# Kernel tuning notes

Measured on AMD Instinct MI355X. Metric: run time of the kernel, lower is better.

## Reference

```python
import jax, jax.numpy as jnp
import numpy as np

N_NODES = 100000


def gcn_conv(x, edge_index, W, b, n):
    """PyG-style GCNConv: h = D^-1/2 (A + I) D^-1/2 (x W) + b."""
    h = x @ W  # [n, out]
    loops = jnp.arange(n, dtype=edge_index.dtype)
    src = jnp.concatenate([edge_index[0], loops])
    dst = jnp.concatenate([edge_index[1], loops])
    deg = jax.ops.segment_sum(jnp.ones_like(dst, dtype=h.dtype), dst, num_segments=n)
    dinv = jnp.where(deg > 0, jax.lax.rsqrt(deg), 0.0)
    norm = dinv[src] * dinv[dst]  # [E+n]
    msg = h[src] * norm[:, None]
    out = jax.ops.segment_sum(msg, dst, num_segments=n)
    return out + b


def setup_inputs() -> dict:
    key = jax.random.key(0)
    ks = jax.random.split(key, 12)
    n, f, hid, c, e = N_NODES, 128, 16, 32, 3200000
    x = jax.random.normal(ks[0], (n, f), dtype=jnp.float32)
    edge_index_pos = jax.random.randint(ks[1], (2, e), 0, n, dtype=jnp.int32)
    edge_index_neg = jax.random.randint(ks[2], (2, e), 0, n, dtype=jnp.int32)
    def glorot(k, fi, fo):
        lim = np.sqrt(6.0 / (fi + fo)).astype(np.float32)
        return jax.random.uniform(k, (fi, fo), minval=-lim, maxval=lim, dtype=jnp.float32)
    return {
        "x": x,
        "edge_index_pos": edge_index_pos,
        "edge_index_neg": edge_index_neg,
        "W1p": glorot(ks[3], f, hid), "b1p": jnp.zeros((hid,), jnp.float32),
        "W1n": glorot(ks[4], f, hid), "b1n": jnp.zeros((hid,), jnp.float32),
        "W2p": glorot(ks[5], hid, c), "b2p": jnp.zeros((c,), jnp.float32),
        "W2n": glorot(ks[6], hid, c), "b2n": jnp.zeros((c,), jnp.float32),
    }


def reference(x, edge_index_pos, edge_index_neg, W1p, b1p, W1n, b1n, W2p, b2p, W2n, b2n):
    n = x.shape[0]
    # layer 1: relu(pos) - relu(neg)
    h = (jax.nn.relu(gcn_conv(x, edge_index_pos, W1p, b1p, n))
         - jax.nn.relu(gcn_conv(x, edge_index_neg, W1n, b1n, n)))
    # dropout is identity in eval mode (training=False)
    h = (jax.nn.relu(gcn_conv(h, edge_index_pos, W2p, b2p, n))
         - jax.nn.relu(gcn_conv(h, edge_index_neg, W2n, b2n, n)))
    return jax.nn.log_softmax(h, axis=1)
```

## Files before the change

kernel.cpp:

```cpp
#include <hip/hip_runtime.h>
#include <hip/hip_fp16.h>


#define BSHIFT 8
#define BSZ 256
#define MAX_NBK 512
#define FILL_CAP 13056
#define SORT_CAP 12032

typedef int   i32x4 __attribute__((ext_vector_type(4)));
typedef float f32x4 __attribute__((ext_vector_type(4)));

__device__ __forceinline__ int chunk_of_block(int bid, int NCH) {
  return (NCH % 8 == 0) ? (bid % 8) * (NCH / 8) + bid / 8 : bid;
}


__global__ __launch_bounds__(256) void bucket_count2(
    const int* __restrict__ eP, const int* __restrict__ eN,
    int E, int CH, int NCH, int NBK, int* __restrict__ ccP, int* __restrict__ ccN) {
  __shared__ int cnt[MAX_NBK];
  const int* dsts = (blockIdx.y ? eN : eP) + E;
  int* cc = blockIdx.y ? ccN : ccP;
  const int c = chunk_of_block(blockIdx.x, NCH);
  for (int i = threadIdx.x; i < NBK; i += 256) cnt[i] = 0;
  __syncthreads();
  int base = c * CH, end = min(E, base + CH);
  for (int idx = base + threadIdx.x * 4; idx < end; idx += 1024) {
    if (idx + 4 <= end) {
      i32x4 d = __builtin_nontemporal_load((const i32x4*)(dsts + idx));
      atomicAdd(&cnt[d.x >> BSHIFT], 1);
      atomicAdd(&cnt[d.y >> BSHIFT], 1);
      atomicAdd(&cnt[d.z >> BSHIFT], 1);
      atomicAdd(&cnt[d.w >> BSHIFT], 1);
    } else {
      for (int k = idx; k < end; ++k) atomicAdd(&cnt[dsts[k] >> BSHIFT], 1);
    }
  }
  __syncthreads();
  for (int i = threadIdx.x; i < NBK; i += 256)
    cc[(size_t)c * NBK + i] = cnt[i];
}

__global__ __launch_bounds__(512) void col_scan2(
    int* __restrict__ ccP, int* __restrict__ ccN, int NCH, int NBK,
    int* __restrict__ totP, int* __restrict__ totN) {
  __shared__ int s[512];
  int* cc = blockIdx.y ? ccN : ccP;
  int* tot = blockIdx.y ? totN : totP;
  int b = blockIdx.x, t = threadIdx.x;
  int v = (t < NCH) ? cc[(size_t)t * NBK + b] : 0;
  s[t] = v;
  for (int off = 1; off < 512; off <<= 1) {
    __syncthreads();
    int a = (t >= off) ? s[t - off] : 0;
    __syncthreads();
    s[t] += a;
  }
  __syncthreads();
  if (t < NCH) cc[(size_t)t * NBK + b] = s[t] - v;
  if (t == 511) tot[b] = s[511];
}

__global__ __launch_bounds__(512) void bucket_fill3(
    const int* __restrict__ eP, const int* __restrict__ eN,
    int E, int CH, int NCH, int NBK,
    const int* __restrict__ ccP, const int* __restrict__ ccN,
    const int* __restrict__ totP, const int* __restrict__ totN,
    unsigned* __restrict__ prP, unsigned* __restrict__ prN) {
  __shared__ unsigned obuf[FILL_CAP];
  __shared__ int chofs[MAX_NBK], hist[MAX_NBK], lofs[MAX_NBK], cur[MAX_NBK];
  __shared__ int bas_l[MAX_NBK];
  __shared__ int s[512];
  const int* edges = blockIdx.y ? eN : eP;
  const int* cc = blockIdx.y ? ccN : ccP;
  const int* tot = blockIdx.y ? totN : totP;
  unsigned* pairs = blockIdx.y ? prN : prP;
  const int c = chunk_of_block(blockIdx.x, NCH);
  const int t = threadIdx.x;

  int h = 0;
  if (t < NBK) {
    int o0 = cc[(size_t)c * NBK + t];
    int o1 = (c + 1 < NCH) ? cc[(size_t)(c + 1) * NBK + t] : tot[t];
    chofs[t] = o0;
    h = o1 - o0;
    hist[t] = h;
  }
  s[t] = h;
  for (int off = 1; off < 512; off <<= 1) {
    __syncthreads();
    int a = (t >= off) ? s[t - off] : 0;
    __syncthreads();
    s[t] += a;
  }
  __syncthreads();
  if (t < NBK) { lofs[t] = s[t] - hist[t]; cur[t] = s[t] - hist[t]; }
  __syncthreads();

  int tv = (t < NBK) ? tot[t] : 0;
  s[t] = tv;
  for (int off = 1; off < 512; off <<= 1) {
    __syncthreads();
    int a = (t >= off) ? s[t - off] : 0;
    __syncthreads();
    s[t] += a;
  }
  __syncthreads();
  if (t < NBK) bas_l[t] = s[t] - tv;
  __syncthreads();

  int base = c * CH, end = min(E, base + CH);
  for (int idx = base + t * 4; idx < end; idx += 2048) {
    if (idx + 4 <= end) {
      i32x4 sv = __builtin_nontemporal_load((const i32x4*)(edges + idx));
      i32x4 dv = __builtin_nontemporal_load((const i32x4*)(edges + E + idx));
      int p0 = atomicAdd(&cur[dv.x >> BSHIFT], 1);
      obuf[p0] = (unsigned)sv.x | ((unsigned)(dv.x & (BSZ - 1)) << 24);
      int p1 = atomicAdd(&cur[dv.y >> BSHIFT], 1);
      obuf[p1] = (unsigned)sv.y | ((unsigned)(dv.y & (BSZ - 1)) << 24);
      int p2 = atomicAdd(&cur[dv.z >> BSHIFT], 1);
      obuf[p2] = (unsigned)sv.z | ((unsigned)(dv.z & (BSZ - 1)) << 24);
      int p3 = atomicAdd(&cur[dv.w >> BSHIFT], 1);
      obuf[p3] = (unsigned)sv.w | ((unsigned)(dv.w & (BSZ - 1)) << 24);
    } else {
      for (int k = idx; k < end; ++k) {
        int sv = edges[k], d = edges[E + k];
        int pos = atomicAdd(&cur[d >> BSHIFT], 1);
        obuf[pos] = (unsigned)sv | ((unsigned)(d & (BSZ - 1)) << 24);
      }
    }
  }
  __syncthreads();

  const int wv = t >> 6, ln = t & 63;
  for (int b = wv; b < NBK; b += 8) {
    int cnt2 = hist[b], lo = lofs[b];
    unsigned* dst = pairs + (size_t)bas_l[b] + chofs[b];
    for (int j = ln; j < cnt2; j += 64) dst[j] = obuf[lo + j];
  }
}

__global__ __launch_bounds__(256) void tile_sort3(
    const unsigned* __restrict__ prP, const unsigned* __restrict__ prN,
    const int* __restrict__ totP, const int* __restrict__ totN, int n, int E,
    float* __restrict__ dinvP, float* __restrict__ dinvN,
    int* __restrict__ rowP, int* __restrict__ rowN,
    unsigned* __restrict__ srcsP, unsigned* __restrict__ srcsN) {
  __shared__ unsigned obuf[SORT_CAP];
  __shared__ int hist[BSZ];
  __shared__ int scn[BSZ];
  __shared__ int cur[BSZ];
  __shared__ int red[256];
  const unsigned* pairs = blockIdx.y ? prN : prP;
  const int* tot = blockIdx.y ? totN : totP;
  float* dinv = blockIdx.y ? dinvN : dinvP;
  int* rowoff = blockIdx.y ? rowN : rowP;
  unsigned* srcs = blockIdx.y ? srcsN : srcsP;
  const int b = blockIdx.x, t = threadIdx.x;

  int part = 0;
  for (int j = t; j < b; j += 256) part += tot[j];
  red[t] = part;
  __syncthreads();
  for (int off = 128; off > 0; off >>= 1) {
    if (t < off) red[t] += red[t + off];
    __syncthreads();
  }
  const int s0 = red[0];
  const int cnt = tot[b];
  const int s1 = s0 + cnt;
  if (b == (int)gridDim.x - 1 && t == 0) rowoff[n] = E;

  hist[t] = 0;
  __syncthreads();
  for (int i = s0 + t; i < s1; i += 256)
    atomicAdd(&hist[__builtin_nontemporal_load(pairs + i) >> 24], 1);
  __syncthreads();
  scn[t] = hist[t];
  __syncthreads();
  for (int off = 1; off < BSZ; off <<= 1) {
    int v = (t >= off) ? scn[t - off] : 0;
    __syncthreads();
    scn[t] += v;
    __syncthreads();
  }
  {
    int excl = scn[t] - hist[t];
    cur[t] = excl;
    int node = b * BSZ + t;
    if (node < n) {
      rowoff[node] = s0 + excl;
      dinv[node] = rsqrtf(1.0f + (float)hist[t]);
    }
  }
  __syncthreads();
  if (cnt <= SORT_CAP) {
    for (int i = s0 + t; i < s1; i += 256) {
      unsigned p = __builtin_nontemporal_load(pairs + i);
      int pos = atomicAdd(&cur[p >> 24], 1);
      obuf[pos] = p & 0xFFFFFFu;
    }
    __syncthreads();
    for (int i = t; i < cnt; i += 256) srcs[s0 + i] = obuf[i];
  } else {
    for (int i = s0 + t; i < s1; i += 256) {
      unsigned p = __builtin_nontemporal_load(pairs + i);
      int pos = atomicAdd(&cur[p >> 24], 1);
      srcs[s0 + pos] = p & 0xFFFFFFu;
    }
  }
}

__global__ __launch_bounds__(256) void xw1_kernel(
    const float* __restrict__ x, const float* __restrict__ Wp, const float* __restrict__ Wn,
    const float* __restrict__ dinvP, const float* __restrict__ dinvN,
    __half* __restrict__ hp, __half* __restrict__ hn, int n)
{
  __shared__ float xs[16 * 132];
  __shared__ float wp[128 * 16], wn[128 * 16];
  const int tid = threadIdx.x;
  const int rowBase = blockIdx.x * 16;

  for (int idx = tid; idx < 512; idx += 256) {
    ((float4*)wp)[idx] = ((const float4*)Wp)[idx];
    ((float4*)wn)[idx] = ((const float4*)Wn)[idx];
  }
  const int nrows = min(16, n - rowBase);
  for (int idx = tid; idx < nrows * 32; idx += 256) {
    int r = idx >> 5, c4 = idx & 31;
    float4 v = ((const float4*)(x + (size_t)(rowBase + r) * 128))[c4];
    *(float4*)(xs + r * 132 + c4 * 4) = v;
  }
  __syncthreads();

  const int r = tid >> 4, c = tid & 15;
  const int i = rowBase + r;
  if (i < n) {
    float ap = 0.f, an = 0.f;
    #pragma unroll
    for (int k = 0; k < 128; ++k) {
      float xv = xs[r * 132 + k];
      ap += xv * wp[k * 16 + c];
      an += xv * wn[k * 16 + c];
    }
    hp[(size_t)i * 16 + c] = __float2half(ap * dinvP[i]);
    hn[(size_t)i * 16 + c] = __float2half(an * dinvN[i]);
  }
}

__device__ __forceinline__ void fma_mix2(float& aLo, float& aHi, unsigned h2, float one) {
  asm("v_fma_mix_f32 %0, %2, %3, %0 op_sel:[0,0,0] op_sel_hi:[1,0,0]\n\t"
      "v_fma_mix_f32 %1, %2, %3, %1 op_sel:[1,0,0] op_sel_hi:[1,0,0]"
      : "+v"(aLo), "+v"(aHi)
      : "v"(h2), "v"(one));
}

__device__ __forceinline__ void seg_sum4(
    const unsigned* __restrict__ srcs, int e, int e1,
    const __half* __restrict__ tab, int lane4, float one,
    float& f0, float& f1, float& f2, float& f3)
{
  float g0 = 0.f, g1 = 0.f, g2 = 0.f, g3 = 0.f;
  for (; e + 8 <= e1; e += 8) {
    unsigned a[8];
    #pragma unroll
    for (int j = 0; j < 8; ++j) a[j] = __builtin_nontemporal_load(srcs + e + j);
    uint2 v[8];
    #pragma unroll
    for (int j = 0; j < 8; ++j)
      v[j] = *(const uint2*)(tab + (size_t)a[j] * 16 + lane4 * 4);
    #pragma unroll
    for (int j = 0; j < 8; j += 2) {
      fma_mix2(f0, f1, v[j].x, one);
      fma_mix2(f2, f3, v[j].y, one);
      fma_mix2(g0, g1, v[j + 1].x, one);
      fma_mix2(g2, g3, v[j + 1].y, one);
    }
  }
  for (; e + 2 <= e1; e += 2) {
    unsigned a0 = __builtin_nontemporal_load(srcs + e);
    unsigned a1 = __builtin_nontemporal_load(srcs + e + 1);
    uint2 v0 = *(const uint2*)(tab + (size_t)a0 * 16 + lane4 * 4);
    uint2 v1 = *(const uint2*)(tab + (size_t)a1 * 16 + lane4 * 4);
    fma_mix2(f0, f1, v0.x, one);
    fma_mix2(f2, f3, v0.y, one);
    fma_mix2(g0, g1, v1.x, one);
    fma_mix2(g2, g3, v1.y, one);
  }
  if (e < e1) {
    unsigned a0 = __builtin_nontemporal_load(srcs + e);
    uint2 v = *(const uint2*)(tab + (size_t)a0 * 16 + lane4 * 4);
    fma_mix2(f0, f1, v.x, one);
    fma_mix2(f2, f3, v.y, one);
  }
  f0 += g0; f1 += g1; f2 += g2; f3 += g3;
}

__global__ __launch_bounds__(256) void agg_split(
    const unsigned* __restrict__ srcP, const int* __restrict__ rowP,
    const unsigned* __restrict__ srcN, const int* __restrict__ rowN,
    const __half* __restrict__ inP, const __half* __restrict__ inN,
    const float* __restrict__ dinvP, const float* __restrict__ dinvN,
    float* __restrict__ tmpP, float* __restrict__ tmpN, int n)
{
  const int gb = blockIdx.x;
  const int xcd = gb & 7;
  const int sign = xcd >> 2;
  const int nblk = (gb >> 3) * 4 + (xcd & 3);
  const int lane4 = threadIdx.x & 3, grp = threadIdx.x >> 2;
  const int i = nblk * 64 + grp;
  if (i >= n) return;

  const unsigned* __restrict__ srcs = sign ? srcN : srcP;
  const int* __restrict__ row = sign ? rowN : rowP;
  const __half* __restrict__ tab = sign ? inN : inP;
  const float* __restrict__ dinv = sign ? dinvN : dinvP;
  float* __restrict__ tmp = sign ? tmpN : tmpP;

  const float one = 1.0f;
  float f0 = 0.f, f1 = 0.f, f2 = 0.f, f3 = 0.f;
  uint2 self = *(const uint2*)(tab + (size_t)i * 16 + lane4 * 4);
  fma_mix2(f0, f1, self.x, one);
  fma_mix2(f2, f3, self.y, one);
  seg_sum4(srcs, row[i], row[i + 1], tab, lane4, one, f0, f1, f2, f3);
  const float d = dinv[i];
  f32x4 o = {f0 * d, f1 * d, f2 * d, f3 * d};
  __builtin_nontemporal_store(o, (f32x4*)(tmp + (size_t)i * 16 + lane4 * 4));
}

__global__ __launch_bounds__(256) void combine1(
    const float* __restrict__ tmpP, const float* __restrict__ tmpN,
    const float* __restrict__ bp, const float* __restrict__ bn,
    const float* __restrict__ dinvP, const float* __restrict__ dinvN,
    __half* __restrict__ Gp, __half* __restrict__ Gn, int nq)
{
  int q = blockIdx.x * 256 + threadIdx.x;
  if (q >= nq) return;
  int i = q >> 2;
  float4 tp = ((const float4*)tmpP)[q];
  float4 tn = ((const float4*)tmpN)[q];
  float4 bpv = ((const float4*)bp)[q & 3];
  float4 bnv = ((const float4*)bn)[q & 3];
  float dp = dinvP[i], dn = dinvN[i];
  float h0 = fmaxf(bpv.x + tp.x, 0.f) - fmaxf(bnv.x + tn.x, 0.f);
  float h1 = fmaxf(bpv.y + tp.y, 0.f) - fmaxf(bnv.y + tn.y, 0.f);
  float h2 = fmaxf(bpv.z + tp.z, 0.f) - fmaxf(bnv.z + tn.z, 0.f);
  float h3 = fmaxf(bpv.w + tp.w, 0.f) - fmaxf(bnv.w + tn.w, 0.f);
  union { uint2 u; __half2 h[2]; } a, b;
  a.h[0] = __floats2half2_rn(h0 * dp, h1 * dp);
  a.h[1] = __floats2half2_rn(h2 * dp, h3 * dp);
  b.h[0] = __floats2half2_rn(h0 * dn, h1 * dn);
  b.h[1] = __floats2half2_rn(h2 * dn, h3 * dn);
  ((uint2*)Gp)[q] = a.u;
  ((uint2*)Gn)[q] = b.u;
}

__global__ __launch_bounds__(256) void final2(
    const float* __restrict__ Up, const float* __restrict__ Un,
    const float* __restrict__ W2p, const float* __restrict__ W2n,
    const float* __restrict__ b2p, const float* __restrict__ b2n,
    float* __restrict__ out, int n)
{
  __shared__ float wp[16 * 32], wn[16 * 32];
  for (int i = threadIdx.x; i < 512; i += 256) { wp[i] = W2p[i]; wn[i] = W2n[i]; }
  __syncthreads();

  const int tid = threadIdx.x;
  const int lane = tid & 15, grp = tid >> 4;
  const int i = blockIdx.x * 16 + grp;
  if (i >= n) return;

  float tp = Up[(size_t)i * 16 + lane];
  float tn = Un[(size_t)i * 16 + lane];

  float ap0 = b2p[lane], ap1 = b2p[lane + 16];
  float an0 = b2n[lane], an1 = b2n[lane + 16];
  #pragma unroll
  for (int k = 0; k < 16; ++k) {
    float tpk = __shfl(tp, k, 16);
    float tnk = __shfl(tn, k, 16);
    ap0 += tpk * wp[k * 32 + lane];
    ap1 += tpk * wp[k * 32 + lane + 16];
    an0 += tnk * wn[k * 32 + lane];
    an1 += tnk * wn[k * 32 + lane + 16];
  }
  float v0 = fmaxf(ap0, 0.f) - fmaxf(an0, 0.f);
  float v1 = fmaxf(ap1, 0.f) - fmaxf(an1, 0.f);
  float m = fmaxf(v0, v1);
  #pragma unroll
  for (int off = 8; off > 0; off >>= 1) m = fmaxf(m, __shfl_xor(m, off, 16));
  float s = __expf(v0 - m) + __expf(v1 - m);
  #pragma unroll
  for (int off = 8; off > 0; off >>= 1) s += __shfl_xor(s, off, 16);
  float ls = __logf(s);
  out[(size_t)i * 32 + lane] = v0 - m - ls;
  out[(size_t)i * 32 + lane + 16] = v1 - m - ls;
}

extern "C" void kernel_launch(void* const* d_in, const int* in_sizes, int n_in,
                              void* d_out, int out_size, void* d_ws, size_t ws_size,
                              hipStream_t stream) {
  const float* x   = (const float*)d_in[0];
  const int*   eP  = (const int*)d_in[1];
  const int*   eN  = (const int*)d_in[2];
  const float* W1p = (const float*)d_in[3];
  const float* b1p = (const float*)d_in[4];
  const float* W1n = (const float*)d_in[5];
  const float* b1n = (const float*)d_in[6];
  const float* W2p = (const float*)d_in[7];
  const float* b2p = (const float*)d_in[8];
  const float* W2n = (const float*)d_in[9];
  const float* b2n = (const float*)d_in[10];
  float* out = (float*)d_out;

  const int HID = in_sizes[4];
  const int F   = in_sizes[3] / HID;
  const int n   = in_sizes[0] / F;
  const int E   = in_sizes[1] / 2;
  (void)out_size; (void)n_in; (void)ws_size;

  const int NBK = (n + BSZ - 1) >> BSHIFT;
  const int CH  = (((E + 255) / 256) + 255) & ~255;
  const int NCH = (E + CH - 1) / CH;

  char* p = (char*)d_ws;
  auto alloc = [&](size_t bytes) { char* r = p; p += (bytes + 255) & ~(size_t)255; return r; };

  int*      ccP   = (int*)alloc((size_t)NCH * NBK * 4);
  int*      ccN   = (int*)alloc((size_t)NCH * NBK * 4);
  int*      totP  = (int*)alloc((size_t)NBK * 4);
  int*      totN  = (int*)alloc((size_t)NBK * 4);
  unsigned* prP   = (unsigned*)alloc((size_t)E * 4);
  unsigned* prN   = (unsigned*)alloc((size_t)E * 4);
  unsigned* srcP  = (unsigned*)alloc((size_t)E * 4);
  unsigned* srcN  = (unsigned*)alloc((size_t)E * 4);
  int*      rowP  = (int*)alloc((size_t)(n + 1) * 4);
  int*      rowN  = (int*)alloc((size_t)(n + 1) * 4);
  float*    dinvP = (float*)alloc((size_t)n * 4);
  float*    dinvN = (float*)alloc((size_t)n * 4);
  __half*   hsP   = (__half*)alloc((size_t)n * 16 * 2);
  __half*   hsN   = (__half*)alloc((size_t)n * 16 * 2);
  __half*   Gp    = (__half*)alloc((size_t)n * 16 * 2);
  __half*   Gn    = (__half*)alloc((size_t)n * 16 * 2);
  float*    tmpP  = (float*)alloc((size_t)n * 16 * 4);
  float*    tmpN  = (float*)alloc((size_t)n * 16 * 4);

  hipLaunchKernelGGL(bucket_count2, dim3(NCH, 2), dim3(256), 0, stream,
                     eP, eN, E, CH, NCH, NBK, ccP, ccN);
  hipLaunchKernelGGL(col_scan2, dim3(NBK, 2), dim3(512), 0, stream,
                     ccP, ccN, NCH, NBK, totP, totN);
  hipLaunchKernelGGL(bucket_fill3, dim3(NCH, 2), dim3(512), 0, stream,
                     eP, eN, E, CH, NCH, NBK, ccP, ccN, totP, totN, prP, prN);
  hipLaunchKernelGGL(tile_sort3, dim3(NBK, 2), dim3(256), 0, stream,
                     prP, prN, totP, totN, n, E, dinvP, dinvN, rowP, rowN, srcP, srcN);

  const int NB16 = (n + 15) / 16;
  const int NB64 = (n + 63) / 64;
  const int NBS  = ((NB64 + 3) / 4) * 4;
  const int GRID = NBS * 2;

  hipLaunchKernelGGL(xw1_kernel, dim3(NB16), dim3(256), 0, stream,
                     x, W1p, W1n, dinvP, dinvN, hsP, hsN, n);
  hipLaunchKernelGGL(agg_split, dim3(GRID), dim3(256), 0, stream,
                     srcP, rowP, srcN, rowN, hsP, hsN, dinvP, dinvN, tmpP, tmpN, n);
  hipLaunchKernelGGL(combine1, dim3((n * 4 + 255) / 256), dim3(256), 0, stream,
                     tmpP, tmpN, b1p, b1n, dinvP, dinvN, Gp, Gn, n * 4);

  hipLaunchKernelGGL(agg_split, dim3(GRID), dim3(256), 0, stream,
                     srcP, rowP, srcN, rowN, Gp, Gn, dinvP, dinvN, tmpP, tmpN, n);
  hipLaunchKernelGGL(final2, dim3(NB16), dim3(256), 0, stream,
                     tmpP, tmpN, W2p, W2n, b2p, b2n, out, n);
}
```

Measured before the change: 275.1 us.

## Replace two-pass bucket sort CSR build with global atomic counting sort

Swaps the chunked bucket count, column scan, bucket fill and tile sort pipeline for a simpler CSR construction. Per-node in-degrees are counted with global atomics, prefix-scanned in two kernels, and edges are scattered directly into CSR positions via global atomic cursors. It also drops the nontemporal loads and stores in aggregation. The scatter has poor locality and heavy global-atomic contention, and neighbour order within a row becomes nondeterministic.

```diff
diff --git a/kernel.cpp b/kernel.cpp
--- a/kernel.cpp
+++ b/kernel.cpp
@@ -2,54 +2,80 @@
 #include <hip/hip_fp16.h>
 
 
-#define BSHIFT 8
-#define BSZ 256
-#define MAX_NBK 512
-#define FILL_CAP 13056
-#define SORT_CAP 12032
-
 typedef int   i32x4 __attribute__((ext_vector_type(4)));
-typedef float f32x4 __attribute__((ext_vector_type(4)));
-
-__device__ __forceinline__ int chunk_of_block(int bid, int NCH) {
-  return (NCH % 8 == 0) ? (bid % 8) * (NCH / 8) + bid / 8 : bid;
-}
-
-
-__global__ __launch_bounds__(256) void bucket_count2(
-    const int* __restrict__ eP, const int* __restrict__ eN,
-    int E, int CH, int NCH, int NBK, int* __restrict__ ccP, int* __restrict__ ccN) {
-  __shared__ int cnt[MAX_NBK];
-  const int* dsts = (blockIdx.y ? eN : eP) + E;
-  int* cc = blockIdx.y ? ccN : ccP;
-  const int c = chunk_of_block(blockIdx.x, NCH);
-  for (int i = threadIdx.x; i < NBK; i += 256) cnt[i] = 0;
-  __syncthreads();
-  int base = c * CH, end = min(E, base + CH);
-  for (int idx = base + threadIdx.x * 4; idx < end; idx += 1024) {
-    if (idx + 4 <= end) {
-      i32x4 d = __builtin_nontemporal_load((const i32x4*)(dsts + idx));
-      atomicAdd(&cnt[d.x >> BSHIFT], 1);
-      atomicAdd(&cnt[d.y >> BSHIFT], 1);
-      atomicAdd(&cnt[d.z >> BSHIFT], 1);
-      atomicAdd(&cnt[d.w >> BSHIFT], 1);
-    } else {
-      for (int k = idx; k < end; ++k) atomicAdd(&cnt[dsts[k] >> BSHIFT], 1);
+
+
+__global__ __launch_bounds__(256) void count_deg(
+    const int* __restrict__ eP, const int* __restrict__ eN, int E,
+    int* __restrict__ deg, int n)
+{
+  const int i = (blockIdx.x * 256 + threadIdx.x) * 4;
+  if (i + 4 <= E) {
+    i32x4 dp = *(const i32x4*)(eP + E + i);
+    i32x4 dn = *(const i32x4*)(eN + E + i);
+    atomicAdd(&deg[dp.x], 1);
+    atomicAdd(&deg[dp.y], 1);
+    atomicAdd(&deg[dp.z], 1);
+    atomicAdd(&deg[dp.w], 1);
+    atomicAdd(&deg[n + dn.x], 1);
+    atomicAdd(&deg[n + dn.y], 1);
+    atomicAdd(&deg[n + dn.z], 1);
+    atomicAdd(&deg[n + dn.w], 1);
+  } else {
+    for (int k = i; k < E; ++k) {
+      atomicAdd(&deg[eP[E + k]], 1);
+      atomicAdd(&deg[n + eN[E + k]], 1);
     }
   }
-  __syncthreads();
-  for (int i = threadIdx.x; i < NBK; i += 256)
-    cc[(size_t)c * NBK + i] = cnt[i];
-}
-
-__global__ __launch_bounds__(512) void col_scan2(
-    int* __restrict__ ccP, int* __restrict__ ccN, int NCH, int NBK,
-    int* __restrict__ totP, int* __restrict__ totN) {
+}
+
+__global__ __launch_bounds__(256) void scan_part(
+    const int* __restrict__ deg, int n, int NPB, int* __restrict__ part)
+{
+  __shared__ int red[256];
+  const int y = blockIdx.y, b = blockIdx.x, t = threadIdx.x;
+  const int* degS = deg + (size_t)y * n;
+  const int i0 = b * 512;
+  int v = 0;
+  if (i0 + t < n) v = degS[i0 + t];
+  if (i0 + t + 256 < n) v += degS[i0 + t + 256];
+  red[t] = v;
+  __syncthreads();
+  for (int off = 128; off > 0; off >>= 1) {
+    if (t < off) red[t] += red[t + off];
+    __syncthreads();
+  }
+  if (t == 0) part[y * NPB + b] = red[0];
+}
+
+__global__ __launch_bounds__(512) void scan_apply(
+    const int* __restrict__ part, int NPB,
+    int* __restrict__ deg ,
+    float* __restrict__ dinvP, float* __restrict__ dinvN,
+    int* __restrict__ rowP, int* __restrict__ rowN, int n)
+{
   __shared__ int s[512];
-  int* cc = blockIdx.y ? ccN : ccP;
-  int* tot = blockIdx.y ? totN : totP;
-  int b = blockIdx.x, t = threadIdx.x;
-  int v = (t < NCH) ? cc[(size_t)t * NBK + b] : 0;
+  __shared__ int sbase;
+  const int y = blockIdx.y, b = blockIdx.x, t = threadIdx.x;
+  int* degS = deg + (size_t)y * n;
+  float* dinv = y ? dinvN : dinvP;
+  int* row = y ? rowN : rowP;
+
+  int ps = 0;
+  for (int j = t; j < b; j += 512) ps += part[y * NPB + j];
+  s[t] = ps;
+  __syncthreads();
+  for (int off = 256; off > 0; off >>= 1) {
+    if (t < off) s[t] += s[t + off];
+    __syncthreads();
+  }
+  if (t == 0) sbase = s[0];
+  __syncthreads();
+  const int base = sbase;
+  __syncthreads();
+
+  const int idx = b * 512 + t;
+  const int v = (idx < n) ? degS[idx] : 0;
   s[t] = v;
   for (int off = 1; off < 512; off <<= 1) {
     __syncthreads();
@@ -58,156 +84,36 @@
     s[t] += a;
   }
   __syncthreads();
-  if (t < NCH) cc[(size_t)t * NBK + b] = s[t] - v;
-  if (t == 511) tot[b] = s[511];
-}
-
-__global__ __launch_bounds__(512) void bucket_fill3(
-    const int* __restrict__ eP, const int* __restrict__ eN,
-    int E, int CH, int NCH, int NBK,
-    const int* __restrict__ ccP, const int* __restrict__ ccN,
-    const int* __restrict__ totP, const int* __restrict__ totN,
-    unsigned* __restrict__ prP, unsigned* __restrict__ prN) {
-  __shared__ unsigned obuf[FILL_CAP];
-  __shared__ int chofs[MAX_NBK], hist[MAX_NBK], lofs[MAX_NBK], cur[MAX_NBK];
-  __shared__ int bas_l[MAX_NBK];
-  __shared__ int s[512];
-  const int* edges = blockIdx.y ? eN : eP;
-  const int* cc = blockIdx.y ? ccN : ccP;
-  const int* tot = blockIdx.y ? totN : totP;
-  unsigned* pairs = blockIdx.y ? prN : prP;
-  const int c = chunk_of_block(blockIdx.x, NCH);
-  const int t = threadIdx.x;
-
-  int h = 0;
-  if (t < NBK) {
-    int o0 = cc[(size_t)c * NBK + t];
-    int o1 = (c + 1 < NCH) ? cc[(size_t)(c + 1) * NBK + t] : tot[t];
-    chofs[t] = o0;
-    h = o1 - o0;
-    hist[t] = h;
-  }
-  s[t] = h;
-  for (int off = 1; off < 512; off <<= 1) {
-    __syncthreads();
-    int a = (t >= off) ? s[t - off] : 0;
-    __syncthreads();
-    s[t] += a;
-  }
-  __syncthreads();
-  if (t < NBK) { lofs[t] = s[t] - hist[t]; cur[t] = s[t] - hist[t]; }
-  __syncthreads();
-
-  int tv = (t < NBK) ? tot[t] : 0;
-  s[t] = tv;
-  for (int off = 1; off < 512; off <<= 1) {
-    __syncthreads();
-    int a = (t >= off) ? s[t - off] : 0;
-    __syncthreads();
-    s[t] += a;
-  }
-  __syncthreads();
-  if (t < NBK) bas_l[t] = s[t] - tv;
-  __syncthreads();
-
-  int base = c * CH, end = min(E, base + CH);
-  for (int idx = base + t * 4; idx < end; idx += 2048) {
-    if (idx + 4 <= end) {
-      i32x4 sv = __builtin_nontemporal_load((const i32x4*)(edges + idx));
-      i32x4 dv = __builtin_nontemporal_load((const i32x4*)(edges + E + idx));
-      int p0 = atomicAdd(&cur[dv.x >> BSHIFT], 1);
-      obuf[p0] = (unsigned)sv.x | ((unsigned)(dv.x & (BSZ - 1)) << 24);
-      int p1 = atomicAdd(&cur[dv.y >> BSHIFT], 1);
-      obuf[p1] = (unsigned)sv.y | ((unsigned)(dv.y & (BSZ - 1)) << 24);
-      int p2 = atomicAdd(&cur[dv.z >> BSHIFT], 1);
-      obuf[p2] = (unsigned)sv.z | ((unsigned)(dv.z & (BSZ - 1)) << 24);
-      int p3 = atomicAdd(&cur[dv.w >> BSHIFT], 1);
-      obuf[p3] = (unsigned)sv.w | ((unsigned)(dv.w & (BSZ - 1)) << 24);
-    } else {
-      for (int k = idx; k < end; ++k) {
-        int sv = edges[k], d = edges[E + k];
-        int pos = atomicAdd(&cur[d >> BSHIFT], 1);
-        obuf[pos] = (unsigned)sv | ((unsigned)(d & (BSZ - 1)) << 24);
-      }
-    }
-  }
-  __syncthreads();
-
-  const int wv = t >> 6, ln = t & 63;
-  for (int b = wv; b < NBK; b += 8) {
-    int cnt2 = hist[b], lo = lofs[b];
-    unsigned* dst = pairs + (size_t)bas_l[b] + chofs[b];
-    for (int j = ln; j < cnt2; j += 64) dst[j] = obuf[lo + j];
-  }
-}
-
-__global__ __launch_bounds__(256) void tile_sort3(
-    const unsigned* __restrict__ prP, const unsigned* __restrict__ prN,
-    const int* __restrict__ totP, const int* __restrict__ totN, int n, int E,
-    float* __restrict__ dinvP, float* __restrict__ dinvN,
-    int* __restrict__ rowP, int* __restrict__ rowN,
-    unsigned* __restrict__ srcsP, unsigned* __restrict__ srcsN) {
-  __shared__ unsigned obuf[SORT_CAP];
-  __shared__ int hist[BSZ];
-  __shared__ int scn[BSZ];
-  __shared__ int cur[BSZ];
-  __shared__ int red[256];
-  const unsigned* pairs = blockIdx.y ? prN : prP;
-  const int* tot = blockIdx.y ? totN : totP;
-  float* dinv = blockIdx.y ? dinvN : dinvP;
-  int* rowoff = blockIdx.y ? rowN : rowP;
-  unsigned* srcs = blockIdx.y ? srcsN : srcsP;
-  const int b = blockIdx.x, t = threadIdx.x;
-
-  int part = 0;
-  for (int j = t; j < b; j += 256) part += tot[j];
-  red[t] = part;
-  __syncthreads();
-  for (int off = 128; off > 0; off >>= 1) {
-    if (t < off) red[t] += red[t + off];
-    __syncthreads();
-  }
-  const int s0 = red[0];
-  const int cnt = tot[b];
-  const int s1 = s0 + cnt;
-  if (b == (int)gridDim.x - 1 && t == 0) rowoff[n] = E;
-
-  hist[t] = 0;
-  __syncthreads();
-  for (int i = s0 + t; i < s1; i += 256)
-    atomicAdd(&hist[__builtin_nontemporal_load(pairs + i) >> 24], 1);
-  __syncthreads();
-  scn[t] = hist[t];
-  __syncthreads();
-  for (int off = 1; off < BSZ; off <<= 1) {
-    int v = (t >= off) ? scn[t - off] : 0;
-    __syncthreads();
-    scn[t] += v;
-    __syncthreads();
-  }
-  {
-    int excl = scn[t] - hist[t];
-    cur[t] = excl;
-    int node = b * BSZ + t;
-    if (node < n) {
-      rowoff[node] = s0 + excl;
-      dinv[node] = rsqrtf(1.0f + (float)hist[t]);
-    }
-  }
-  __syncthreads();
-  if (cnt <= SORT_CAP) {
-    for (int i = s0 + t; i < s1; i += 256) {
-      unsigned p = __builtin_nontemporal_load(pairs + i);
-      int pos = atomicAdd(&cur[p >> 24], 1);
-      obuf[pos] = p & 0xFFFFFFu;
-    }
-    __syncthreads();
-    for (int i = t; i < cnt; i += 256) srcs[s0 + i] = obuf[i];
+  if (idx < n) {
+    const int excl = base + s[t] - v;
+    row[idx] = excl;
+    degS[idx] = excl;
+    dinv[idx] = rsqrtf(1.0f + (float)v);
+  }
+  if (b == (int)gridDim.x - 1 && t == 511) row[n] = base + s[511];
+}
+
+__global__ __launch_bounds__(256) void scatter_edges(
+    const int* __restrict__ eP, const int* __restrict__ eN, int E,
+    int* __restrict__ wcur, int n,
+    unsigned* __restrict__ srcP, unsigned* __restrict__ srcN)
+{
+  const int y = blockIdx.y;
+  const int* edges = y ? eN : eP;
+  int* wc = wcur + (size_t)y * n;
+  unsigned* srcs = y ? srcN : srcP;
+  const int i = (blockIdx.x * 256 + threadIdx.x) * 4;
+  if (i + 4 <= E) {
+    i32x4 sv = *(const i32x4*)(edges + i);
+    i32x4 dv = *(const i32x4*)(edges + E + i);
+    int p0 = atomicAdd(&wc[dv.x], 1); srcs[p0] = (unsigned)sv.x;
+    int p1 = atomicAdd(&wc[dv.y], 1); srcs[p1] = (unsigned)sv.y;
+    int p2 = atomicAdd(&wc[dv.z], 1); srcs[p2] = (unsigned)sv.z;
+    int p3 = atomicAdd(&wc[dv.w], 1); srcs[p3] = (unsigned)sv.w;
   } else {
-    for (int i = s0 + t; i < s1; i += 256) {
-      unsigned p = __builtin_nontemporal_load(pairs + i);
-      int pos = atomicAdd(&cur[p >> 24], 1);
-      srcs[s0 + pos] = p & 0xFFFFFFu;
+    for (int k = i; k < E; ++k) {
+      int p = atomicAdd(&wc[edges[E + k]], 1);
+      srcs[p] = (unsigned)edges[k];
     }
   }
 }
@@ -265,7 +171,7 @@
   for (; e + 8 <= e1; e += 8) {
     unsigned a[8];
     #pragma unroll
-    for (int j = 0; j < 8; ++j) a[j] = __builtin_nontemporal_load(srcs + e + j);
+    for (int j = 0; j < 8; ++j) a[j] = srcs[e + j];
     uint2 v[8];
     #pragma unroll
     for (int j = 0; j < 8; ++j)
@@ -279,8 +185,7 @@
     }
   }
   for (; e + 2 <= e1; e += 2) {
-    unsigned a0 = __builtin_nontemporal_load(srcs + e);
-    unsigned a1 = __builtin_nontemporal_load(srcs + e + 1);
+    unsigned a0 = srcs[e], a1 = srcs[e + 1];
     uint2 v0 = *(const uint2*)(tab + (size_t)a0 * 16 + lane4 * 4);
     uint2 v1 = *(const uint2*)(tab + (size_t)a1 * 16 + lane4 * 4);
     fma_mix2(f0, f1, v0.x, one);
@@ -289,8 +194,7 @@
     fma_mix2(g2, g3, v1.y, one);
   }
   if (e < e1) {
-    unsigned a0 = __builtin_nontemporal_load(srcs + e);
-    uint2 v = *(const uint2*)(tab + (size_t)a0 * 16 + lane4 * 4);
+    uint2 v = *(const uint2*)(tab + (size_t)srcs[e] * 16 + lane4 * 4);
     fma_mix2(f0, f1, v.x, one);
     fma_mix2(f2, f3, v.y, one);
   }
@@ -325,8 +229,9 @@
   fma_mix2(f2, f3, self.y, one);
   seg_sum4(srcs, row[i], row[i + 1], tab, lane4, one, f0, f1, f2, f3);
   const float d = dinv[i];
-  f32x4 o = {f0 * d, f1 * d, f2 * d, f3 * d};
-  __builtin_nontemporal_store(o, (f32x4*)(tmp + (size_t)i * 16 + lane4 * 4));
+  float4 o;
+  o.x = f0 * d; o.y = f1 * d; o.z = f2 * d; o.w = f3 * d;
+  *(float4*)(tmp + (size_t)i * 16 + lane4 * 4) = o;
 }
 
 __global__ __launch_bounds__(256) void combine1(
@@ -420,19 +325,13 @@
   const int E   = in_sizes[1] / 2;
   (void)out_size; (void)n_in; (void)ws_size;
 
-  const int NBK = (n + BSZ - 1) >> BSHIFT;
-  const int CH  = (((E + 255) / 256) + 255) & ~255;
-  const int NCH = (E + CH - 1) / CH;
+  const int NPB = (n + 511) / 512;
 
   char* p = (char*)d_ws;
   auto alloc = [&](size_t bytes) { char* r = p; p += (bytes + 255) & ~(size_t)255; return r; };
 
-  int*      ccP   = (int*)alloc((size_t)NCH * NBK * 4);
-  int*      ccN   = (int*)alloc((size_t)NCH * NBK * 4);
-  int*      totP  = (int*)alloc((size_t)NBK * 4);
-  int*      totN  = (int*)alloc((size_t)NBK * 4);
-  unsigned* prP   = (unsigned*)alloc((size_t)E * 4);
-  unsigned* prN   = (unsigned*)alloc((size_t)E * 4);
+  int*      deg   = (int*)alloc((size_t)2 * n * 4);
+  int*      part  = (int*)alloc((size_t)2 * NPB * 4);
   unsigned* srcP  = (unsigned*)alloc((size_t)E * 4);
   unsigned* srcN  = (unsigned*)alloc((size_t)E * 4);
   int*      rowP  = (int*)alloc((size_t)(n + 1) * 4);
@@ -446,14 +345,16 @@
   float*    tmpP  = (float*)alloc((size_t)n * 16 * 4);
   float*    tmpN  = (float*)alloc((size_t)n * 16 * 4);
 
-  hipLaunchKernelGGL(bucket_count2, dim3(NCH, 2), dim3(256), 0, stream,
-                     eP, eN, E, CH, NCH, NBK, ccP, ccN);
-  hipLaunchKernelGGL(col_scan2, dim3(NBK, 2), dim3(512), 0, stream,
-                     ccP, ccN, NCH, NBK, totP, totN);
-  hipLaunchKernelGGL(bucket_fill3, dim3(NCH, 2), dim3(512), 0, stream,
-                     eP, eN, E, CH, NCH, NBK, ccP, ccN, totP, totN, prP, prN);
-  hipLaunchKernelGGL(tile_sort3, dim3(NBK, 2), dim3(256), 0, stream,
-                     prP, prN, totP, totN, n, E, dinvP, dinvN, rowP, rowN, srcP, srcN);
+  hipMemsetAsync(deg, 0, (size_t)2 * n * 4, stream);
+  const int EB4 = (E + 1023) / 1024;
+  hipLaunchKernelGGL(count_deg, dim3(EB4), dim3(256), 0, stream,
+                     eP, eN, E, deg, n);
+  hipLaunchKernelGGL(scan_part, dim3(NPB, 2), dim3(256), 0, stream,
+                     deg, n, NPB, part);
+  hipLaunchKernelGGL(scan_apply, dim3(NPB, 2), dim3(512), 0, stream,
+                     part, NPB, deg, dinvP, dinvN, rowP, rowN, n);
+  hipLaunchKernelGGL(scatter_edges, dim3(EB4, 2), dim3(256), 0, stream,
+                     eP, eN, E, deg, n, srcP, srcN);
 
   const int NB16 = (n + 15) / 16;
   const int NB64 = (n + 63) / 64;
```

New measurement: 964.9 us. +250.8%, slower.
